# Performance work log

Hardware: AMD Instinct MI355X
Metric: run time of the kernel (lower is better)

## Reference

```python
import jax, jax.numpy as jnp
import numpy as np

N, E = 50000, 640000
IN, HD, OUT, NCLS = 768, 128, 128, 2
H, C = 4, 32  # heads, per-head channels (HD/H = OUT/H = 32)
NEG_SLOPE = 0.2


def _glorot(key, shape):
    fan_in, fan_out = shape[0], shape[1]
    lim = jnp.sqrt(6.0 / (fan_in + fan_out))
    return jax.random.uniform(key, shape, jnp.float32, -lim, lim)


def setup_inputs() -> dict:
    key = jax.random.key(0)
    ks = jax.random.split(key, 24)
    x = jax.random.normal(ks[0], (1, N, IN), jnp.float32)
    edge_index = jax.random.randint(ks[1], (2, E), 0, N, jnp.int64)
    d = {"x": x, "edge_index": edge_index}
    ins = [IN, HD, HD, HD]
    for i in range(4):
        d[f"Wl{i+1}"] = _glorot(ks[2 + 5 * i], (ins[i], H * C))
        d[f"Wr{i+1}"] = _glorot(ks[3 + 5 * i], (ins[i], H * C))
        d[f"att{i+1}"] = _glorot(ks[4 + 5 * i], (H, C))
        d[f"b{i+1}"] = jnp.zeros((H * C,), jnp.float32)
    d["clfW"] = _glorot(ks[22], (OUT, NCLS))
    d["clfb"] = jnp.zeros((NCLS,), jnp.float32)
    return d


def _gatv2_layer(x, Wl, Wr, att, b, src, dst):
    # x: [N, F_in] -> out: [N, H*C]. GATv2: e = a^T LeakyReLU(xl_j + xr_i)
    xl = (x @ Wl).reshape(N, H, C)
    xr = (x @ Wr).reshape(N, H, C)
    h = xl[src] + xr[dst]                                   # [E', H, C] per-edge gather
    e = jnp.einsum('ehc,hc->eh', jax.nn.leaky_relu(h, NEG_SLOPE), att)
    m = jax.ops.segment_max(e, dst, num_segments=N)          # scatter-softmax (stable)
    a = jnp.exp(e - m[dst])
    s = jax.ops.segment_sum(a, dst, num_segments=N)
    alpha = a / (s[dst] + 1e-16)
    out = jax.ops.segment_sum(alpha[..., None] * xl[src], dst, num_segments=N)
    return out.reshape(N, H * C) + b


def reference(x, edge_index, Wl1, Wr1, att1, b1, Wl2, Wr2, att2, b2,
              Wl3, Wr3, att3, b3, Wl4, Wr4, att4, b4, clfW, clfb):
    xn = x.reshape(N, IN)  # torch.squeeze
    loops = jnp.arange(N, dtype=edge_index.dtype)  # PyG add_self_loops=True
    src = jnp.concatenate([edge_index[0], loops])
    dst = jnp.concatenate([edge_index[1], loops])
    h = jax.nn.relu(_gatv2_layer(xn, Wl1, Wr1, att1, b1, src, dst))
    h = jax.nn.relu(_gatv2_layer(h, Wl2, Wr2, att2, b2, src, dst))
    h = jax.nn.relu(_gatv2_layer(h, Wl3, Wr3, att3, b3, src, dst))
    h = _gatv2_layer(h, Wl4, Wr4, att4, b4, src, dst)        # [N, OUT]
    g = jnp.mean(h, axis=0, keepdims=True)                   # unsqueeze+mean over nodes -> [1, OUT]
    return g @ clfW + clfb                                   # [1, NCLS]
```

## Files before the change

### kernel.cpp

```cpp
#include <hip/hip_runtime.h>
#include <hip/hip_bf16.h>

#define NN 50000
#define EE 640000
#define HC 128
#define NB1 196

typedef short bf16x8 __attribute__((ext_vector_type(8)));
typedef float f32x4 __attribute__((ext_vector_type(4)));
typedef unsigned short u16;

__device__ __forceinline__ u16 f2b(float f) {
    unsigned u = __float_as_uint(f);
    unsigned r = u + 0x7FFFu + ((u >> 16) & 1u);
    return (u16)(r >> 16);
}
__device__ __forceinline__ float b2f(u16 h) {
    return __uint_as_float(((unsigned)h) << 16);
}

__device__ __forceinline__ void gload_lds16(const void* g, void* l) {
    __builtin_amdgcn_global_load_lds((const __attribute__((address_space(1))) void*)g,
                                     (__attribute__((address_space(3))) void*)l, 16, 0, 0);
}

__device__ __forceinline__ float red16(float x) {
    x += __int_as_float(__builtin_amdgcn_update_dpp(0, __float_as_int(x), 0xB1, 0xF, 0xF, true));
    x += __int_as_float(__builtin_amdgcn_update_dpp(0, __float_as_int(x), 0x4E, 0xF, 0xF, true));
    x += __int_as_float(__builtin_amdgcn_update_dpp(0, __float_as_int(x), 0x141, 0xF, 0xF, true));
    x += __int_as_float(__builtin_amdgcn_update_dpp(0, __float_as_int(x), 0x128, 0xF, 0xF, true));
    return x;
}


__global__ void k_count(const int* __restrict__ ei, int* __restrict__ cnt) {
    int e = blockIdx.x * blockDim.x + threadIdx.x;
    if (e < EE) atomicAdd(&cnt[ei[EE + e]], 1);
}

__global__ void k_bsum(const int* __restrict__ cnt, int* __restrict__ bsum) {
    __shared__ int sd[256];
    int b = blockIdx.x, t = threadIdx.x, i = b * 256 + t;
    sd[t] = (i < NN) ? cnt[i] + 1 : 0;
    __syncthreads();
    for (int o = 128; o; o >>= 1) { if (t < o) sd[t] += sd[t + o]; __syncthreads(); }
    if (!t) bsum[b] = sd[0];
}

__global__ void k_bscan(const int* __restrict__ bsum, int* __restrict__ bex,
                        int* __restrict__ offs) {
    __shared__ int sd[256];
    int t = threadIdx.x;
    int v = (t < NB1) ? bsum[t] : 0;
    sd[t] = v; __syncthreads();
    for (int o = 1; o < 256; o <<= 1) {
        int u = (t >= o) ? sd[t - o] : 0;
        __syncthreads(); sd[t] += u; __syncthreads();
    }
    bex[t] = sd[t] - v;
    if (t == NB1 - 1) offs[NN] = sd[t];
}

__global__ void k_offs(const int* __restrict__ cnt_in, const int* __restrict__ bex,
                       int* __restrict__ offs, int* __restrict__ cursor,
                       int* __restrict__ csr) {
    __shared__ int sd[256];
    int b = blockIdx.x, t = threadIdx.x, i = b * 256 + t;
    int v = (i < NN) ? cnt_in[i] + 1 : 0;
    sd[t] = v; __syncthreads();
    for (int o = 1; o < 256; o <<= 1) {
        int u = (t >= o) ? sd[t - o] : 0;
        __syncthreads(); sd[t] += u; __syncthreads();
    }
    if (i < NN) {
        int o = bex[b] + sd[t] - v;
        offs[i] = o;
        csr[o] = i;
        cursor[i] = o + 1;
    }
}

__global__ void k_fill(const int* __restrict__ ei, int* __restrict__ cursor,
                       int* __restrict__ csr) {
    int e = blockIdx.x * blockDim.x + threadIdx.x;
    if (e < EE) {
        int s = ei[e], d = ei[EE + e];
        int pos = atomicAdd(&cursor[d], 1);
        csr[pos] = s;
    }
}


#define WT_L0 196608
#define WT_LX 32768
#define WT_TOT (WT_L0 + 3 * WT_LX)

__global__ void k_castw_all(const float* __restrict__ Wl1, const float* __restrict__ Wr1,
                            const float* __restrict__ Wl2, const float* __restrict__ Wr2,
                            const float* __restrict__ Wl3, const float* __restrict__ Wr3,
                            const float* __restrict__ Wl4, const float* __restrict__ Wr4,
                            u16* __restrict__ WtAll) {
    int gid = blockIdx.x * 256 + threadIdx.x;
    if (gid >= WT_TOT) return;
    const float *Wl, *Wr;
    int idx, K, base;
    if (gid < WT_L0) { Wl = Wl1; Wr = Wr1; idx = gid; K = 768; base = 0; }
    else {
        int r = gid - WT_L0;
        int l = r >> 15; idx = r & (WT_LX - 1); K = 128; base = WT_L0 + l * WT_LX;
        if (l == 0)      { Wl = Wl2; Wr = Wr2; }
        else if (l == 1) { Wl = Wl3; Wr = Wr3; }
        else             { Wl = Wl4; Wr = Wr4; }
    }
    int c = idx / K, k = idx - c * K;
    float v = (c < 128) ? Wl[k * 128 + c] : Wr[k * 128 + (c - 128)];
    WtAll[base + idx] = f2b(v);
}


template<int K, bool F32A>
__global__ __launch_bounds__(512, 4)
void k_gemm(const void* __restrict__ Ag, const u16* __restrict__ Wt,
            u16* __restrict__ xb) {
    __shared__ __align__(16) u16 As[128 * 64];
    __shared__ __align__(16) u16 Bs[256 * 64];
    const int tid = threadIdx.x;
    const int wv = tid >> 6, ln = tid & 63;
    const int wr = wv >> 2, wc = wv & 3;
    const int m0 = blockIdx.x * 128;
    const int lrow = ln & 15, g = ln >> 4;

    f32x4 acc[4][4] = {};

    const float* Af = (const float*)Ag;
    const u16* Ab = (const u16*)Ag;
    const int arow = tid >> 2, aq = tid & 3;
    int arg = m0 + arow; if (arg >= NN) arg = 0;
    float4 ra0, ra1, ra2, ra3;

    if constexpr (F32A) {
        const float* src = Af + (size_t)arg * K + aq * 16;
        ra0 = *(const float4*)(src);
        ra1 = *(const float4*)(src + 4);
        ra2 = *(const float4*)(src + 8);
        ra3 = *(const float4*)(src + 12);
    }

    constexpr int NSTEP = K / 64;
    for (int ks = 0; ks < NSTEP; ++ks) {
        if constexpr (F32A) {
            const int s = arow & 7;
            bf16x8 v0, v1;
            v0[0] = (short)f2b(ra0.x); v0[1] = (short)f2b(ra0.y);
            v0[2] = (short)f2b(ra0.z); v0[3] = (short)f2b(ra0.w);
            v0[4] = (short)f2b(ra1.x); v0[5] = (short)f2b(ra1.y);
            v0[6] = (short)f2b(ra1.z); v0[7] = (short)f2b(ra1.w);
            v1[0] = (short)f2b(ra2.x); v1[1] = (short)f2b(ra2.y);
            v1[2] = (short)f2b(ra2.z); v1[3] = (short)f2b(ra2.w);
            v1[4] = (short)f2b(ra3.x); v1[5] = (short)f2b(ra3.y);
            v1[6] = (short)f2b(ra3.z); v1[7] = (short)f2b(ra3.w);
            *(bf16x8*)&As[arow * 64 + (((aq * 2) ^ s) * 8)] = v0;
            *(bf16x8*)&As[arow * 64 + (((aq * 2 + 1) ^ s) * 8)] = v1;
        } else {
            #pragma unroll
            for (int q = 0; q < 2; ++q) {
                int r8 = (wv * 2 + q) * 8;
                int row = r8 + (ln >> 3);
                int lc = (ln & 7) ^ (row & 7);
                int rg = m0 + row; if (rg >= NN) rg = 0;
                gload_lds16(Ab + (size_t)rg * K + ks * 64 + lc * 8, &As[r8 * 64]);
            }
        }
        #pragma unroll
        for (int q = 0; q < 4; ++q) {
            int r8 = (wv * 4 + q) * 8;
            int row = r8 + (ln >> 3);
            int lc = (ln & 7) ^ (row & 7);
            gload_lds16(Wt + (size_t)row * K + ks * 64 + lc * 8, &Bs[r8 * 64]);
        }
        __syncthreads();

        if constexpr (F32A) {
            if (ks + 1 < NSTEP) {
                const float* src = Af + (size_t)arg * K + (ks + 1) * 64 + aq * 16;
                ra0 = *(const float4*)(src);
                ra1 = *(const float4*)(src + 4);
                ra2 = *(const float4*)(src + 8);
                ra3 = *(const float4*)(src + 12);
            }
        }

        #pragma unroll
        for (int kk = 0; kk < 2; ++kk) {
            bf16x8 af[4], bfr[4];
            #pragma unroll
            for (int f = 0; f < 4; ++f) {
                int r = wr * 64 + f * 16 + lrow;
                af[f] = *(const bf16x8*)&As[r * 64 + (((kk * 4 + g) ^ (r & 7)) * 8)];
                int c = wc * 64 + f * 16 + lrow;
                bfr[f] = *(const bf16x8*)&Bs[c * 64 + (((kk * 4 + g) ^ (c & 7)) * 8)];
            }
            #pragma unroll
            for (int i = 0; i < 4; ++i)
                #pragma unroll
                for (int j = 0; j < 4; ++j)
                    acc[i][j] = __builtin_amdgcn_mfma_f32_16x16x32_bf16(af[i], bfr[j], acc[i][j], 0, 0, 0);
        }
        __syncthreads();
    }

    const int crow0 = m0 + wr * 64 + (g << 2);
    const int ccol0 = wc * 64 + lrow;
    #pragma unroll
    for (int i = 0; i < 4; ++i)
        #pragma unroll
        for (int rr = 0; rr < 4; ++rr) {
            int row = crow0 + i * 16 + rr;
            if (row < NN) {
                #pragma unroll
                for (int j = 0; j < 4; ++j)
                    xb[(size_t)row * 256 + ccol0 + j * 16] = f2b(acc[i][j][rr]);
            }
        }
}


__global__ __launch_bounds__(256)
void k_edge(const u16* __restrict__ xb, const float* __restrict__ att,
            const float* __restrict__ bias, const int* __restrict__ offs,
            const int* __restrict__ csr, u16* __restrict__ outb,
            float* __restrict__ outf, int relu) {
    int i = blockIdx.x * 4 + (threadIdx.x >> 6);
    if (i >= NN) return;
    int ln = threadIdx.x & 63;
    int ch0 = ((ln >> 4) << 5) + ((ln & 15) << 1);

    unsigned xr2 = *(const unsigned*)&xb[(size_t)i * 256 + 128 + ch0];
    float xri0 = b2f((u16)xr2), xri1 = b2f((u16)(xr2 >> 16));
    float2 atv = *(const float2*)&att[ch0];
    const float at0 = atv.x, at1 = atv.y;
    int beg = offs[i];
    int deg = offs[i + 1] - beg;

    float m0v = -3.0e38f, s0v = 0.f, p00 = 0.f, p01 = 0.f;
    float m1v = -3.0e38f, s1v = 0.f, p10 = 0.f, p11 = 0.f;
    float m2v = -3.0e38f, s2v = 0.f, p20 = 0.f, p21 = 0.f;
    float m3v = -3.0e38f, s3v = 0.f, p30 = 0.f, p31 = 0.f;

#define GATH(k, jj) unsigned w##k = *(const unsigned*)&xb[(size_t)(jj) * 256 + ch0];
#define UPD(k, M, S, A0, A1) { \
    float v0 = b2f((u16)w##k), v1 = b2f((u16)(w##k >> 16)); \
    float u0 = v0 + xri0; u0 = (u0 > 0.f) ? u0 : 0.2f * u0; \
    float u1 = v1 + xri1; u1 = (u1 > 0.f) ? u1 : 0.2f * u1; \
    float e = red16(u0 * at0 + u1 * at1); \
    float mn = fmaxf(M, e); float c = __expf(M - mn), ww = __expf(e - mn); \
    S = S * c + ww; A0 = A0 * c + ww * v0; A1 = A1 * c + ww * v1; M = mn; }

    for (int base = 0; base < deg; base += 64) {
        int lim = deg - base; if (lim > 64) lim = 64;
        int idxv = (base + ln < deg) ? csr[beg + base + ln] : 0;
        int p = 0;
        for (; p + 4 <= lim; p += 4) {
            int j0 = __shfl(idxv, p);
            int j1 = __shfl(idxv, p + 1);
            int j2 = __shfl(idxv, p + 2);
            int j3 = __shfl(idxv, p + 3);
            GATH(0, j0) GATH(1, j1) GATH(2, j2) GATH(3, j3)
            UPD(0, m0v, s0v, p00, p01)
            UPD(1, m1v, s1v, p10, p11)
            UPD(2, m2v, s2v, p20, p21)
            UPD(3, m3v, s3v, p30, p31)
        }
        for (; p < lim; ++p) {
            int j0 = __shfl(idxv, p);
            GATH(4, j0)
            UPD(4, m0v, s0v, p00, p01)
        }
    }
#undef GATH
#undef UPD

    float mm = fmaxf(fmaxf(m0v, m1v), fmaxf(m2v, m3v));
    float c0 = __expf(m0v - mm), c1 = __expf(m1v - mm);
    float c2 = __expf(m2v - mm), c3 = __expf(m3v - mm);
    float s = s0v * c0 + s1v * c1 + s2v * c2 + s3v * c3 + 1e-16f;
    float inv = 1.f / s;
    float2 bv = *(const float2*)&bias[ch0];
    float o0 = (p00 * c0 + p10 * c1 + p20 * c2 + p30 * c3) * inv + bv.x;
    float o1 = (p01 * c0 + p11 * c1 + p21 * c2 + p31 * c3) * inv + bv.y;
    if (relu) { o0 = fmaxf(o0, 0.f); o1 = fmaxf(o1, 0.f); }
    if (outb) {
        unsigned pk = (unsigned)f2b(o0) | ((unsigned)f2b(o1) << 16);
        *(unsigned*)&outb[(size_t)i * HC + ch0] = pk;
    }
    if (outf) {
        *(float2*)&outf[(size_t)i * HC + ch0] = make_float2(o0, o1);
    }
}


__global__ __launch_bounds__(256)
void k_colsum(const float* __restrict__ h, float* __restrict__ gsum) {
    __shared__ float4 sd[8][32];
    int t = threadIdx.x;
    int c4 = t & 31, rl = t >> 5;
    float sx = 0.f, sy = 0.f, sz = 0.f, sw = 0.f;
    for (int r = blockIdx.x * 8 + rl; r < NN; r += 8 * gridDim.x) {
        float4 v = *(const float4*)&h[(size_t)r * HC + c4 * 4];
        sx += v.x; sy += v.y; sz += v.z; sw += v.w;
    }
    sd[rl][c4] = make_float4(sx, sy, sz, sw);
    __syncthreads();
    if (rl == 0) {
        float4 a = sd[0][c4];
        #pragma unroll
        for (int q = 1; q < 8; ++q) {
            float4 b = sd[q][c4];
            a.x += b.x; a.y += b.y; a.z += b.z; a.w += b.w;
        }
        atomicAdd(&gsum[c4 * 4 + 0], a.x);
        atomicAdd(&gsum[c4 * 4 + 1], a.y);
        atomicAdd(&gsum[c4 * 4 + 2], a.z);
        atomicAdd(&gsum[c4 * 4 + 3], a.w);
    }
}

__global__ void k_clf(const float* __restrict__ gsum, const float* __restrict__ W,
                      const float* __restrict__ bcls, float* __restrict__ out) {
    __shared__ float v[HC];
    int t = threadIdx.x;
    v[t] = gsum[t] * (1.f / (float)NN);
    __syncthreads();
    if (t < 2) {
        float r = 0.f;
        for (int k = 0; k < HC; ++k) r += v[k] * W[k * 2 + t];
        out[t] = r + bcls[t];
    }
}


extern "C" void kernel_launch(void* const* d_in, const int* in_sizes, int n_in,
                              void* d_out, int out_size, void* d_ws, size_t ws_size,
                              hipStream_t stream) {
    const float* x = (const float*)d_in[0];
    const int* ei = (const int*)d_in[1];
    const float *Wl[4], *Wr[4], *att[4], *bia[4];
    for (int l = 0; l < 4; ++l) {
        Wl[l] = (const float*)d_in[2 + 4 * l];
        Wr[l] = (const float*)d_in[3 + 4 * l];
        att[l] = (const float*)d_in[4 + 4 * l];
        bia[l] = (const float*)d_in[5 + 4 * l];
    }
    const float* clfW = (const float*)d_in[18];
    const float* clfb = (const float*)d_in[19];
    float* outp = (float*)d_out;

    char* w = (char*)d_ws;
    size_t o = 0;
    auto alloc = [&](size_t bytes) {
        char* p = w + o;
        o = (o + bytes + 255) & ~(size_t)255;
        return p;
    };
    int* cnt    = (int*)alloc((size_t)NN * 4);
    float* gsum = (float*)alloc(HC * 4);
    size_t zspan = o;
    int* offs  = (int*)alloc((size_t)(NN + 1) * 4);
    int* csr   = (int*)alloc((size_t)(EE + NN) * 4);
    int* bsum  = (int*)alloc((size_t)NB1 * 4);
    int* bex   = (int*)alloc(256 * 4);
    u16* WtAll = (u16*)alloc((size_t)WT_TOT * 2);
    u16* xb    = (u16*)alloc((size_t)NN * 256 * 2);
    u16* hb0   = (u16*)alloc((size_t)NN * HC * 2);
    u16* hb1   = (u16*)alloc((size_t)NN * HC * 2);
    float* hfin = (float*)alloc((size_t)NN * HC * 4);

    hipMemsetAsync(cnt, 0, zspan, stream);
    k_count<<<(EE + 255) / 256, 256, 0, stream>>>(ei, cnt);
    k_bsum<<<NB1, 256, 0, stream>>>(cnt, bsum);
    k_bscan<<<1, 256, 0, stream>>>(bsum, bex, offs);
    k_offs<<<NB1, 256, 0, stream>>>(cnt, bex, offs, cnt, csr);
    k_fill<<<(EE + 255) / 256, 256, 0, stream>>>(ei, cnt, csr);
    k_castw_all<<<(WT_TOT + 255) / 256, 256, 0, stream>>>(
        Wl[0], Wr[0], Wl[1], Wr[1], Wl[2], Wr[2], Wl[3], Wr[3], WtAll);

    const int GB = (NN + 127) / 128;
    const u16* Wt_l[4] = {WtAll, WtAll + WT_L0, WtAll + WT_L0 + WT_LX,
                          WtAll + WT_L0 + 2 * WT_LX};
    const u16* hb_in = nullptr;
    u16* hbb[2] = {hb0, hb1};
    for (int l = 0; l < 4; ++l) {
        if (l == 0) k_gemm<768, true ><<<GB, 512, 0, stream>>>((const void*)x, Wt_l[0], xb);
        else        k_gemm<128, false><<<GB, 512, 0, stream>>>((const void*)hb_in, Wt_l[l], xb);
        u16* ob = (l < 3) ? hbb[l & 1] : nullptr;
        float* of = (l == 3) ? hfin : nullptr;
        k_edge<<<(NN + 3) / 4, 256, 0, stream>>>(xb, att[l], bia[l], offs, csr, ob, of,
                                                 (l < 3) ? 1 : 0);
        hb_in = ob;
    }

    k_colsum<<<504, 256, 0, stream>>>(hfin, gsum);
    k_clf<<<1, 128, 0, stream>>>(gsum, clfW, clfb, outp);
}
```

Measured before the change: 394.5 us.

## Fold block scan into offsets kernel and widen edge loop to eight gathers

```diff
diff --git a/kernel.cpp b/kernel.cpp
--- a/kernel.cpp
+++ b/kernel.cpp
@@ -47,37 +47,31 @@
     if (!t) bsum[b] = sd[0];
 }
 
-__global__ void k_bscan(const int* __restrict__ bsum, int* __restrict__ bex,
-                        int* __restrict__ offs) {
-    __shared__ int sd[256];
-    int t = threadIdx.x;
-    int v = (t < NB1) ? bsum[t] : 0;
-    sd[t] = v; __syncthreads();
-    for (int o = 1; o < 256; o <<= 1) {
-        int u = (t >= o) ? sd[t - o] : 0;
-        __syncthreads(); sd[t] += u; __syncthreads();
-    }
-    bex[t] = sd[t] - v;
-    if (t == NB1 - 1) offs[NN] = sd[t];
-}
-
-__global__ void k_offs(const int* __restrict__ cnt_in, const int* __restrict__ bex,
+__global__ void k_offs(const int* __restrict__ cnt_in, const int* __restrict__ bsum,
                        int* __restrict__ offs, int* __restrict__ cursor,
                        int* __restrict__ csr) {
+    __shared__ int sb[256];
     __shared__ int sd[256];
     int b = blockIdx.x, t = threadIdx.x, i = b * 256 + t;
+    sb[t] = (t < NB1) ? bsum[t] : 0;
     int v = (i < NN) ? cnt_in[i] + 1 : 0;
-    sd[t] = v; __syncthreads();
+    sd[t] = v;
+    __syncthreads();
     for (int o = 1; o < 256; o <<= 1) {
-        int u = (t >= o) ? sd[t - o] : 0;
-        __syncthreads(); sd[t] += u; __syncthreads();
-    }
+        int u1 = (t >= o) ? sd[t - o] : 0;
+        int u2 = (t >= o) ? sb[t - o] : 0;
+        __syncthreads();
+        sd[t] += u1; sb[t] += u2;
+        __syncthreads();
+    }
+    int bex = (b > 0) ? sb[b - 1] : 0;
     if (i < NN) {
-        int o = bex[b] + sd[t] - v;
+        int o = bex + sd[t] - v;
         offs[i] = o;
         csr[o] = i;
         cursor[i] = o + 1;
     }
+    if (b == NB1 - 1 && t == 0) offs[NN] = sb[NB1 - 1];
 }
 
 __global__ void k_fill(const int* __restrict__ ei, int* __restrict__ cursor,
@@ -246,48 +240,66 @@
     float m1v = -3.0e38f, s1v = 0.f, p10 = 0.f, p11 = 0.f;
     float m2v = -3.0e38f, s2v = 0.f, p20 = 0.f, p21 = 0.f;
     float m3v = -3.0e38f, s3v = 0.f, p30 = 0.f, p31 = 0.f;
+    float m4v = -3.0e38f, s4v = 0.f, p40 = 0.f, p41 = 0.f;
+    float m5v = -3.0e38f, s5v = 0.f, p50 = 0.f, p51 = 0.f;
+    float m6v = -3.0e38f, s6v = 0.f, p60 = 0.f, p61 = 0.f;
+    float m7v = -3.0e38f, s7v = 0.f, p70 = 0.f, p71 = 0.f;
 
 #define GATH(k, jj) unsigned w##k = *(const unsigned*)&xb[(size_t)(jj) * 256 + ch0];
-#define UPD(k, M, S, A0, A1) { \
+#define UPD(k, M, S, A0, A1, ok) { \
     float v0 = b2f((u16)w##k), v1 = b2f((u16)(w##k >> 16)); \
-    float u0 = v0 + xri0; u0 = (u0 > 0.f) ? u0 : 0.2f * u0; \
-    float u1 = v1 + xri1; u1 = (u1 > 0.f) ? u1 : 0.2f * u1; \
+    float u0 = v0 + xri0; u0 = fmaxf(u0, 0.2f * u0); \
+    float u1 = v1 + xri1; u1 = fmaxf(u1, 0.2f * u1); \
     float e = red16(u0 * at0 + u1 * at1); \
-    float mn = fmaxf(M, e); float c = __expf(M - mn), ww = __expf(e - mn); \
-    S = S * c + ww; A0 = A0 * c + ww * v0; A1 = A1 * c + ww * v1; M = mn; }
+    float d = e - M; \
+    float tt = __expf(-fabsf(d)); \
+    bool ng = (d <= 0.f) || (!(ok)); \
+    float c = ng ? 1.f : tt; \
+    float ww = (ok) ? (ng ? tt : 1.f) : 0.f; \
+    M = ng ? M : e; \
+    S = S * c + ww; A0 = A0 * c + ww * v0; A1 = A1 * c + ww * v1; }
 
     for (int base = 0; base < deg; base += 64) {
         int lim = deg - base; if (lim > 64) lim = 64;
-        int idxv = (base + ln < deg) ? csr[beg + base + ln] : 0;
-        int p = 0;
-        for (; p + 4 <= lim; p += 4) {
-            int j0 = __shfl(idxv, p);
+        int idxv = (base + ln < deg) ? csr[beg + base + ln] : i;
+        for (int p = 0; p < lim; p += 8) {
+            int j0 = __shfl(idxv, p + 0);
             int j1 = __shfl(idxv, p + 1);
             int j2 = __shfl(idxv, p + 2);
             int j3 = __shfl(idxv, p + 3);
+            int j4 = __shfl(idxv, p + 4);
+            int j5 = __shfl(idxv, p + 5);
+            int j6 = __shfl(idxv, p + 6);
+            int j7 = __shfl(idxv, p + 7);
             GATH(0, j0) GATH(1, j1) GATH(2, j2) GATH(3, j3)
-            UPD(0, m0v, s0v, p00, p01)
-            UPD(1, m1v, s1v, p10, p11)
-            UPD(2, m2v, s2v, p20, p21)
-            UPD(3, m3v, s3v, p30, p31)
-        }
-        for (; p < lim; ++p) {
-            int j0 = __shfl(idxv, p);
-            GATH(4, j0)
-            UPD(4, m0v, s0v, p00, p01)
+            GATH(4, j4) GATH(5, j5) GATH(6, j6) GATH(7, j7)
+            UPD(0, m0v, s0v, p00, p01, true)
+            UPD(1, m1v, s1v, p10, p11, (p + 1 < lim))
+            UPD(2, m2v, s2v, p20, p21, (p + 2 < lim))
+            UPD(3, m3v, s3v, p30, p31, (p + 3 < lim))
+            UPD(4, m4v, s4v, p40, p41, (p + 4 < lim))
+            UPD(5, m5v, s5v, p50, p51, (p + 5 < lim))
+            UPD(6, m6v, s6v, p60, p61, (p + 6 < lim))
+            UPD(7, m7v, s7v, p70, p71, (p + 7 < lim))
         }
     }
 #undef GATH
 #undef UPD
 
-    float mm = fmaxf(fmaxf(m0v, m1v), fmaxf(m2v, m3v));
+    float mm = fmaxf(fmaxf(fmaxf(m0v, m1v), fmaxf(m2v, m3v)),
+                     fmaxf(fmaxf(m4v, m5v), fmaxf(m6v, m7v)));
     float c0 = __expf(m0v - mm), c1 = __expf(m1v - mm);
     float c2 = __expf(m2v - mm), c3 = __expf(m3v - mm);
-    float s = s0v * c0 + s1v * c1 + s2v * c2 + s3v * c3 + 1e-16f;
+    float c4 = __expf(m4v - mm), c5 = __expf(m5v - mm);
+    float c6 = __expf(m6v - mm), c7 = __expf(m7v - mm);
+    float s = s0v * c0 + s1v * c1 + s2v * c2 + s3v * c3
+            + s4v * c4 + s5v * c5 + s6v * c6 + s7v * c7 + 1e-16f;
     float inv = 1.f / s;
     float2 bv = *(const float2*)&bias[ch0];
-    float o0 = (p00 * c0 + p10 * c1 + p20 * c2 + p30 * c3) * inv + bv.x;
-    float o1 = (p01 * c0 + p11 * c1 + p21 * c2 + p31 * c3) * inv + bv.y;
+    float o0 = (p00 * c0 + p10 * c1 + p20 * c2 + p30 * c3
+              + p40 * c4 + p50 * c5 + p60 * c6 + p70 * c7) * inv + bv.x;
+    float o1 = (p01 * c0 + p11 * c1 + p21 * c2 + p31 * c3
+              + p41 * c4 + p51 * c5 + p61 * c6 + p71 * c7) * inv + bv.y;
     if (relu) { o0 = fmaxf(o0, 0.f); o1 = fmaxf(o1, 0.f); }
     if (outb) {
         unsigned pk = (unsigned)f2b(o0) | ((unsigned)f2b(o1) << 16);
@@ -368,7 +380,6 @@
     int* offs  = (int*)alloc((size_t)(NN + 1) * 4);
     int* csr   = (int*)alloc((size_t)(EE + NN) * 4);
     int* bsum  = (int*)alloc((size_t)NB1 * 4);
-    int* bex   = (int*)alloc(256 * 4);
     u16* WtAll = (u16*)alloc((size_t)WT_TOT * 2);
     u16* xb    = (u16*)alloc((size_t)NN * 256 * 2);
     u16* hb0   = (u16*)alloc((size_t)NN * HC * 2);
@@ -378,8 +389,7 @@
     hipMemsetAsync(cnt, 0, zspan, stream);
     k_count<<<(EE + 255) / 256, 256, 0, stream>>>(ei, cnt);
     k_bsum<<<NB1, 256, 0, stream>>>(cnt, bsum);
-    k_bscan<<<1, 256, 0, stream>>>(bsum, bex, offs);
-    k_offs<<<NB1, 256, 0, stream>>>(cnt, bex, offs, cnt, csr);
+    k_offs<<<NB1, 256, 0, stream>>>(cnt, bsum, offs, cnt, csr);
     k_fill<<<(EE + 255) / 256, 256, 0, stream>>>(ei, cnt, csr);
     k_castw_all<<<(WT_TOT + 255) / 256, 256, 0, stream>>>(
         Wl[0], Wr[0], Wl[1], Wr[1], Wl[2], Wr[2], Wl[3], Wr[3], WtAll);
```

After: 460.7 us. +16.8%, slower.
